# Performance work log

Measured on AMD Instinct MI355X. Metric: run time of the kernel, lower is better.

The kernel has to match this reference:

```python
import jax, jax.numpy as jnp
import numpy as np

B, N, D, H = 8, 8192, 512, 8  # batch, seq, hidden, heads
DH = D // H


def _rope_tables(n, d, dtype=jnp.float32):
    # standard rotate-half RoPE tables over the full hidden dim (d/2 freq pairs)
    half = d // 2
    inv_freq = 1.0 / (10000.0 ** (np.arange(0, half, dtype=np.float32) / half))
    pos = np.arange(n, dtype=np.float32)
    ang = np.einsum('n,f->nf', pos, inv_freq)          # [N, D/2]
    ang = np.concatenate([ang, ang], axis=-1)          # [N, D]
    return jnp.asarray(np.cos(ang), dtype), jnp.asarray(np.sin(ang), dtype)


def setup_inputs() -> dict:
    key = jax.random.key(0)
    k1, k2 = jax.random.split(key)
    hidden_states = jax.random.normal(k1, (B, N, D), dtype=jnp.float32)
    num_layers = 24
    std = 0.02 / np.sqrt(2.0 * num_layers * D)
    W = jax.random.normal(k2, (D, D), dtype=jnp.float32) * std
    cos, sin = _rope_tables(N, D)
    return {"hidden_states": hidden_states, "W": W, "cos": cos, "sin": sin}


def _rotate_half(x):
    x1, x2 = jnp.split(x, 2, axis=-1)
    return jnp.concatenate([-x2, x1], axis=-1)


def reference(hidden_states, W, cos, sin):
    # dropout(p=0) in eval mode -> identity
    x = hidden_states * cos + _rotate_half(hidden_states) * sin  # RoPE, [B,N,D]
    q = jnp.einsum('bnd,ed->bne', x, W)                          # F.linear(x, W)
    qh = q.reshape(B, N, H, DH)
    xh = x.reshape(B, N, H, DH)
    # linear-complexity path: (K^T V) then Q @ (.), per head
    kv = jnp.einsum('bnhd,bnhe->bhde', xh, xh)   # [B,H,DH,DH]
    out = jnp.einsum('bnhd,bhde->bnhe', qh, kv)  # [B,N,H,DH]
    return out.reshape(B, N, D)
```

## Files before the change

### kernel.cpp

```cpp
#include <hip/hip_runtime.h>
#include <hip/hip_bf16.h>
#include <stdint.h>

#define BB 8
#define NN 8192
#define DD 512
#define HH 8
#define DHD 64

typedef __attribute__((ext_vector_type(8))) short bf16x8;
typedef __attribute__((ext_vector_type(4))) float f32x4;

__device__ __forceinline__ unsigned short f2bf(float f) {
  union { float f; unsigned int u; } v; v.f = f;
  return (unsigned short)((v.u + 0x7FFFu + ((v.u >> 16) & 1u)) >> 16);
}

__device__ __forceinline__ void async16(const void* g, void* l) {
  __builtin_amdgcn_global_load_lds(
      (const __attribute__((address_space(1))) void*)g,
      (__attribute__((address_space(3))) void*)l, 16, 0, 0);
}

__global__ void rope_kernel(const float* __restrict__ h, const float* __restrict__ cs,
                            const float* __restrict__ sn, unsigned short* __restrict__ x) {
  int t = blockIdx.x * 256 + threadIdx.x;
  int r = t >> 6;
  int c = (t & 63) << 2;
  int n = r & (NN - 1);
  size_t base  = (size_t)r * DD + c;
  size_t tbase = (size_t)n * DD + c;
  float4 h1 = *(const float4*)(h + base);
  float4 h2 = *(const float4*)(h + base + 256);
  float4 c1 = *(const float4*)(cs + tbase);
  float4 c2 = *(const float4*)(cs + tbase + 256);
  float4 s1 = *(const float4*)(sn + tbase);
  float4 s2 = *(const float4*)(sn + tbase + 256);
  float4 x1, x2;
  x1.x = h1.x * c1.x - h2.x * s1.x;  x2.x = h2.x * c2.x + h1.x * s2.x;
  x1.y = h1.y * c1.y - h2.y * s1.y;  x2.y = h2.y * c2.y + h1.y * s2.y;
  x1.z = h1.z * c1.z - h2.z * s1.z;  x2.z = h2.z * c2.z + h1.z * s2.z;
  x1.w = h1.w * c1.w - h2.w * s1.w;  x2.w = h2.w * c2.w + h1.w * s2.w;
  uint2 p1, p2;
  p1.x = (unsigned)f2bf(x1.x) | ((unsigned)f2bf(x1.y) << 16);
  p1.y = (unsigned)f2bf(x1.z) | ((unsigned)f2bf(x1.w) << 16);
  p2.x = (unsigned)f2bf(x2.x) | ((unsigned)f2bf(x2.y) << 16);
  p2.y = (unsigned)f2bf(x2.z) | ((unsigned)f2bf(x2.w) << 16);
  *(uint2*)(x + base)       = p1;
  *(uint2*)(x + base + 256) = p2;
}

__global__ void kv_kernel(const unsigned short* __restrict__ x, float* __restrict__ kv) {
  __shared__ __align__(16) unsigned short xt[64 * 72];
  int bh = blockIdx.x;
  int b = bh >> 3, hh = bh & 7;
  int chunk = blockIdx.y;
  int rows_per_chunk = NN / gridDim.y;
  int tiles = rows_per_chunk >> 6;
  int tid = threadIdx.x;
  int wave = tid >> 6, lane = tid & 63;
  int d0 = (wave & 1) * 32, e0 = (wave >> 1) * 32;
  int l15 = lane & 15, q = lane >> 4;
  f32x4 acc[2][2];
#pragma unroll
  for (int i = 0; i < 2; ++i)
#pragma unroll
    for (int j = 0; j < 2; ++j) acc[i][j] = (f32x4){0.f, 0.f, 0.f, 0.f};

  int nrow = tid >> 2;
  int cseg = (tid & 3) * 16;
  const unsigned short* srcbase = x + (size_t)b * NN * DD + hh * DHD + cseg;

  for (int t = 0; t < tiles; ++t) {
    int n0 = chunk * rows_per_chunk + t * 64;
    const unsigned short* src = srcbase + (size_t)(n0 + nrow) * DD;
    uint4 p0 = *(const uint4*)(src);
    uint4 p1 = *(const uint4*)(src + 8);
    unsigned short v[16];
    *(uint4*)&v[0] = p0;  *(uint4*)&v[8] = p1;
#pragma unroll
    for (int j = 0; j < 16; ++j) xt[(cseg + j) * 72 + nrow] = v[j];
    __syncthreads();
#pragma unroll
    for (int ks = 0; ks < 64; ks += 32) {
      bf16x8 a0 = *(const bf16x8*)&xt[(d0 + l15) * 72 + ks + q * 8];
      bf16x8 a1 = *(const bf16x8*)&xt[(d0 + 16 + l15) * 72 + ks + q * 8];
      bf16x8 b0 = *(const bf16x8*)&xt[(e0 + l15) * 72 + ks + q * 8];
      bf16x8 b1 = *(const bf16x8*)&xt[(e0 + 16 + l15) * 72 + ks + q * 8];
      acc[0][0] = __builtin_amdgcn_mfma_f32_16x16x32_bf16(a0, b0, acc[0][0], 0, 0, 0);
      acc[1][0] = __builtin_amdgcn_mfma_f32_16x16x32_bf16(a1, b0, acc[1][0], 0, 0, 0);
      acc[0][1] = __builtin_amdgcn_mfma_f32_16x16x32_bf16(a0, b1, acc[0][1], 0, 0, 0);
      acc[1][1] = __builtin_amdgcn_mfma_f32_16x16x32_bf16(a1, b1, acc[1][1], 0, 0, 0);
    }
    __syncthreads();
  }
  float* dst = kv + (size_t)bh * 4096;
#pragma unroll
  for (int i = 0; i < 2; ++i)
#pragma unroll
    for (int j = 0; j < 2; ++j) {
      int col = e0 + j * 16 + l15;
#pragma unroll
      for (int reg = 0; reg < 4; ++reg) {
        int row = d0 + i * 16 + q * 4 + reg;
        atomicAdd(&dst[row * 64 + col], acc[i][j][reg]);
      }
    }
}

__global__ void wkvt_kernel(const float* __restrict__ W, const float* __restrict__ kv,
                            unsigned short* __restrict__ wkvt) {
  __shared__ float kvs[4096];
  __shared__ float ws[8192];
  int bh = blockIdx.x, fc = blockIdx.y;
  int b = bh >> 3, hh = bh & 7;
  int f0 = fc * 128;
  int tid = threadIdx.x;
#pragma unroll
  for (int i = 0; i < 4; ++i) {
    int idx = i * 1024 + tid * 4;
    *(float4*)&kvs[idx] = *(const float4*)&kv[(size_t)bh * 4096 + idx];
  }
#pragma unroll
  for (int i = 0; i < 8; ++i) {
    int idx = i * 1024 + tid * 4;
    int d = idx >> 7, f = idx & 127;
    *(float4*)&ws[idx] = *(const float4*)&W[(size_t)(hh * DHD + d) * DD + f0 + f];
  }
  __syncthreads();
  int e = tid & 63, fg = tid >> 6;
  float acc[32];
#pragma unroll
  for (int j = 0; j < 32; ++j) acc[j] = 0.f;
  for (int d = 0; d < 64; ++d) {
    float kvv = kvs[d * 64 + e];
    const float* wr = &ws[d * 128 + fg * 32];
#pragma unroll
    for (int j = 0; j < 32; ++j) acc[j] = fmaf(wr[j], kvv, acc[j]);
  }
  unsigned short tmp[32];
#pragma unroll
  for (int j = 0; j < 32; ++j) tmp[j] = f2bf(acc[j]);
  size_t obase = ((size_t)(b * DD + hh * DHD + e)) * DD + f0 + fg * 32;
#pragma unroll
  for (int qq = 0; qq < 4; ++qq)
    *(uint4*)&wkvt[obase + qq * 8] = *(uint4*)&tmp[qq * 8];
}

__global__ __launch_bounds__(256) void gemm_kernel(const unsigned short* __restrict__ x,
                                                   const unsigned short* __restrict__ wkvt,
                                                   float* __restrict__ out) {
  __shared__ __align__(16) unsigned short As[128 * 64];
  __shared__ __align__(16) unsigned short Bs[128 * 64];
  int mt = blockIdx.x, ct = blockIdx.y, bz = blockIdx.z;
  int tid = threadIdx.x, wave = tid >> 6, lane = tid & 63;
  int m_off = (wave & 1) * 64, c_off = (wave >> 1) * 64;
  int l15 = lane & 15, q = lane >> 4;
  int lrow = lane >> 3, lcol = (lane & 7) * 8;
  const unsigned short* Ag = x    + ((size_t)bz * NN + mt * 128) * DD;
  const unsigned short* Bg = wkvt + ((size_t)bz * DD + ct * 128) * DD;
  f32x4 acc[4][4];
#pragma unroll
  for (int i = 0; i < 4; ++i)
#pragma unroll
    for (int j = 0; j < 4; ++j) acc[i][j] = (f32x4){0.f, 0.f, 0.f, 0.f};

  for (int kk = 0; kk < 512; kk += 64) {
#pragma unroll
    for (int i = 0; i < 4; ++i) {
      int r = wave * 32 + i * 8 + lrow;
      async16(Ag + (size_t)r * DD + kk + lcol, &As[(wave * 32 + i * 8) * 64]);
      async16(Bg + (size_t)r * DD + kk + lcol, &Bs[(wave * 32 + i * 8) * 64]);
    }
    __syncthreads();
#pragma unroll
    for (int ks = 0; ks < 64; ks += 32) {
      bf16x8 a[4], bb[4];
#pragma unroll
      for (int i = 0; i < 4; ++i)
        a[i] = *(const bf16x8*)&As[(m_off + i * 16 + l15) * 64 + ks + q * 8];
#pragma unroll
      for (int j = 0; j < 4; ++j)
        bb[j] = *(const bf16x8*)&Bs[(c_off + j * 16 + l15) * 64 + ks + q * 8];
#pragma unroll
      for (int i = 0; i < 4; ++i)
#pragma unroll
        for (int j = 0; j < 4; ++j)
          acc[i][j] = __builtin_amdgcn_mfma_f32_16x16x32_bf16(a[i], bb[j], acc[i][j], 0, 0, 0);
    }
    __syncthreads();
  }
  float* ob = out + ((size_t)bz * NN + mt * 128) * DD + ct * 128;
#pragma unroll
  for (int i = 0; i < 4; ++i)
#pragma unroll
    for (int j = 0; j < 4; ++j) {
      int row = m_off + i * 16 + q * 4;
      int col = c_off + j * 16 + l15;
#pragma unroll
      for (int reg = 0; reg < 4; ++reg)
        ob[(size_t)(row + reg) * DD + col] = acc[i][j][reg];
    }
}

extern "C" void kernel_launch(void* const* d_in, const int* in_sizes, int n_in,
                              void* d_out, int out_size, void* d_ws, size_t ws_size,
                              hipStream_t stream) {
  (void)in_sizes; (void)n_in; (void)out_size;
  const float* h  = (const float*)d_in[0];
  const float* W  = (const float*)d_in[1];
  const float* cs = (const float*)d_in[2];
  const float* sn = (const float*)d_in[3];
  float* out = (float*)d_out;

  const size_t x_full     = (size_t)BB * NN * DD * 2;
  const size_t kv_full    = (size_t)BB * HH * DHD * DHD * 4;
  const size_t wkvt_full  = (size_t)BB * DD * DD * 2;
  const size_t x_batch    = (size_t)NN * DD * 2;
  const size_t kv_batch   = (size_t)HH * DHD * DHD * 4;
  const size_t wkvt_batch = (size_t)DD * DD * 2;

  if (ws_size >= x_full + kv_full + wkvt_full) {
    unsigned short* xw   = (unsigned short*)d_ws;
    float*          kv   = (float*)((char*)d_ws + x_full);
    unsigned short* wkvt = (unsigned short*)((char*)d_ws + x_full + kv_full);
    hipMemsetAsync(kv, 0, kv_full, stream);
    rope_kernel<<<dim3(BB * NN * 64 / 256), dim3(256), 0, stream>>>(h, cs, sn, xw);
    kv_kernel<<<dim3(BB * HH, 8), dim3(256), 0, stream>>>(xw, kv);
    wkvt_kernel<<<dim3(BB * HH, 4), dim3(256), 0, stream>>>(W, kv, wkvt);
    gemm_kernel<<<dim3(NN / 128, DD / 128, BB), dim3(256), 0, stream>>>(xw, wkvt, out);
  } else {
    unsigned short* xw   = (unsigned short*)d_ws;
    float*          kv   = (float*)((char*)d_ws + x_batch);
    unsigned short* wkvt = (unsigned short*)((char*)d_ws + x_batch + kv_batch);
    for (int b = 0; b < BB; ++b) {
      hipMemsetAsync(kv, 0, kv_batch, stream);
      rope_kernel<<<dim3(NN * 64 / 256), dim3(256), 0, stream>>>(
          h + (size_t)b * NN * DD, cs, sn, xw);
      kv_kernel<<<dim3(HH, 32), dim3(256), 0, stream>>>(xw, kv);
      wkvt_kernel<<<dim3(HH, 4), dim3(256), 0, stream>>>(W, kv, wkvt);
      gemm_kernel<<<dim3(NN / 128, DD / 128, 1), dim3(256), 0, stream>>>(
          xw, wkvt, out + (size_t)b * NN * DD);
    }
  }
}
```

Measured before the change: 337.6 us.

## Replace KV atomics with partial buffers, widen GEMM tile, nontemporal RoPE loads

The KV reduction now writes per-chunk partial sums to a buffer, and the next kernel adds them up. This replaces the atomicAdd calls and the memset. The KV transpose staging is rebuilt to pack pairs of rows into 32-bit LDS stores with a new padding. The GEMM tile is widened to 128x256 with 32 accumulators per wave, which cuts repeated A-tile loads at the cost of register pressure and occupancy. RoPE uses nontemporal loads for the hidden-state input and vector arithmetic.

```diff
diff --git a/kernel.cpp b/kernel.cpp
--- a/kernel.cpp
+++ b/kernel.cpp
@@ -7,9 +7,11 @@
 #define DD 512
 #define HH 8
 #define DHD 64
+#define NCH 16
 
 typedef __attribute__((ext_vector_type(8))) short bf16x8;
 typedef __attribute__((ext_vector_type(4))) float f32x4;
+typedef __attribute__((ext_vector_type(4))) float f4v;
 
 __device__ __forceinline__ unsigned short f2bf(float f) {
   union { float f; unsigned int u; } v; v.f = f;
@@ -30,17 +32,14 @@
   int n = r & (NN - 1);
   size_t base  = (size_t)r * DD + c;
   size_t tbase = (size_t)n * DD + c;
-  float4 h1 = *(const float4*)(h + base);
-  float4 h2 = *(const float4*)(h + base + 256);
-  float4 c1 = *(const float4*)(cs + tbase);
-  float4 c2 = *(const float4*)(cs + tbase + 256);
-  float4 s1 = *(const float4*)(sn + tbase);
-  float4 s2 = *(const float4*)(sn + tbase + 256);
-  float4 x1, x2;
-  x1.x = h1.x * c1.x - h2.x * s1.x;  x2.x = h2.x * c2.x + h1.x * s2.x;
-  x1.y = h1.y * c1.y - h2.y * s1.y;  x2.y = h2.y * c2.y + h1.y * s2.y;
-  x1.z = h1.z * c1.z - h2.z * s1.z;  x2.z = h2.z * c2.z + h1.z * s2.z;
-  x1.w = h1.w * c1.w - h2.w * s1.w;  x2.w = h2.w * c2.w + h1.w * s2.w;
+  f4v h1 = __builtin_nontemporal_load((const f4v*)(h + base));
+  f4v h2 = __builtin_nontemporal_load((const f4v*)(h + base + 256));
+  f4v c1 = *(const f4v*)(cs + tbase);
+  f4v c2 = *(const f4v*)(cs + tbase + 256);
+  f4v s1 = *(const f4v*)(sn + tbase);
+  f4v s2 = *(const f4v*)(sn + tbase + 256);
+  f4v x1 = h1 * c1 - h2 * s1;
+  f4v x2 = h2 * c2 + h1 * s2;
   uint2 p1, p2;
   p1.x = (unsigned)f2bf(x1.x) | ((unsigned)f2bf(x1.y) << 16);
   p1.y = (unsigned)f2bf(x1.z) | ((unsigned)f2bf(x1.w) << 16);
@@ -50,13 +49,11 @@
   *(uint2*)(x + base + 256) = p2;
 }
 
-__global__ void kv_kernel(const unsigned short* __restrict__ x, float* __restrict__ kv) {
-  __shared__ __align__(16) unsigned short xt[64 * 72];
+__global__ void kv_kernel(const unsigned short* __restrict__ x, float* __restrict__ kvp) {
+  __shared__ __align__(16) unsigned short xt[64 * 68];
   int bh = blockIdx.x;
   int b = bh >> 3, hh = bh & 7;
   int chunk = blockIdx.y;
-  int rows_per_chunk = NN / gridDim.y;
-  int tiles = rows_per_chunk >> 6;
   int tid = threadIdx.x;
   int wave = tid >> 6, lane = tid & 63;
   int d0 = (wave & 1) * 32, e0 = (wave >> 1) * 32;
@@ -67,34 +64,37 @@
 #pragma unroll
     for (int j = 0; j < 2; ++j) acc[i][j] = (f32x4){0.f, 0.f, 0.f, 0.f};
 
-  int nrow = tid >> 2;
-  int cseg = (tid & 3) * 16;
-  const unsigned short* srcbase = x + (size_t)b * NN * DD + hh * DHD + cseg;
-
-  for (int t = 0; t < tiles; ++t) {
-    int n0 = chunk * rows_per_chunk + t * 64;
-    const unsigned short* src = srcbase + (size_t)(n0 + nrow) * DD;
-    uint4 p0 = *(const uint4*)(src);
-    uint4 p1 = *(const uint4*)(src + 8);
-    unsigned short v[16];
-    *(uint4*)&v[0] = p0;  *(uint4*)&v[8] = p1;
-#pragma unroll
-    for (int j = 0; j < 16; ++j) xt[(cseg + j) * 72 + nrow] = v[j];
+  int rp  = tid & 31;
+  int seg = tid >> 5;
+  const unsigned short* srcbase = x + (size_t)b * NN * DD + hh * DHD + seg * 8;
+
+  for (int t = 0; t < 8; ++t) {
+    int n0 = chunk * 512 + t * 64;
+    const unsigned short* s0 = srcbase + (size_t)(n0 + 2 * rp) * DD;
+    uint4 p0 = *(const uint4*)(s0);
+    uint4 p1 = *(const uint4*)(s0 + DD);
+    unsigned short a0[8], a1[8];
+    *(uint4*)a0 = p0;  *(uint4*)a1 = p1;
+    __syncthreads();
+#pragma unroll
+    for (int j = 0; j < 8; ++j) {
+      unsigned pack = (unsigned)a0[j] | ((unsigned)a1[j] << 16);
+      ((unsigned*)xt)[(seg * 8 + j) * 34 + rp] = pack;
+    }
     __syncthreads();
 #pragma unroll
     for (int ks = 0; ks < 64; ks += 32) {
-      bf16x8 a0 = *(const bf16x8*)&xt[(d0 + l15) * 72 + ks + q * 8];
-      bf16x8 a1 = *(const bf16x8*)&xt[(d0 + 16 + l15) * 72 + ks + q * 8];
-      bf16x8 b0 = *(const bf16x8*)&xt[(e0 + l15) * 72 + ks + q * 8];
-      bf16x8 b1 = *(const bf16x8*)&xt[(e0 + 16 + l15) * 72 + ks + q * 8];
-      acc[0][0] = __builtin_amdgcn_mfma_f32_16x16x32_bf16(a0, b0, acc[0][0], 0, 0, 0);
-      acc[1][0] = __builtin_amdgcn_mfma_f32_16x16x32_bf16(a1, b0, acc[1][0], 0, 0, 0);
-      acc[0][1] = __builtin_amdgcn_mfma_f32_16x16x32_bf16(a0, b1, acc[0][1], 0, 0, 0);
-      acc[1][1] = __builtin_amdgcn_mfma_f32_16x16x32_bf16(a1, b1, acc[1][1], 0, 0, 0);
-    }
-    __syncthreads();
-  }
-  float* dst = kv + (size_t)bh * 4096;
+      bf16x8 a0f = *(const bf16x8*)&xt[(d0 + l15) * 68 + ks + q * 8];
+      bf16x8 a1f = *(const bf16x8*)&xt[(d0 + 16 + l15) * 68 + ks + q * 8];
+      bf16x8 b0f = *(const bf16x8*)&xt[(e0 + l15) * 68 + ks + q * 8];
+      bf16x8 b1f = *(const bf16x8*)&xt[(e0 + 16 + l15) * 68 + ks + q * 8];
+      acc[0][0] = __builtin_amdgcn_mfma_f32_16x16x32_bf16(a0f, b0f, acc[0][0], 0, 0, 0);
+      acc[1][0] = __builtin_amdgcn_mfma_f32_16x16x32_bf16(a1f, b0f, acc[1][0], 0, 0, 0);
+      acc[0][1] = __builtin_amdgcn_mfma_f32_16x16x32_bf16(a0f, b1f, acc[0][1], 0, 0, 0);
+      acc[1][1] = __builtin_amdgcn_mfma_f32_16x16x32_bf16(a1f, b1f, acc[1][1], 0, 0, 0);
+    }
+  }
+  float* dst = kvp + ((size_t)chunk * gridDim.x + bh) * 4096;
 #pragma unroll
   for (int i = 0; i < 2; ++i)
 #pragma unroll
@@ -103,23 +103,27 @@
 #pragma unroll
       for (int reg = 0; reg < 4; ++reg) {
         int row = d0 + i * 16 + q * 4 + reg;
-        atomicAdd(&dst[row * 64 + col], acc[i][j][reg]);
+        dst[row * 64 + col] = acc[i][j][reg];
       }
     }
 }
 
-__global__ void wkvt_kernel(const float* __restrict__ W, const float* __restrict__ kv,
+__global__ void wkvt_kernel(const float* __restrict__ W, const float* __restrict__ kvp,
                             unsigned short* __restrict__ wkvt) {
   __shared__ float kvs[4096];
   __shared__ float ws[8192];
   int bh = blockIdx.x, fc = blockIdx.y;
+  int nbh = gridDim.x;
   int b = bh >> 3, hh = bh & 7;
   int f0 = fc * 128;
   int tid = threadIdx.x;
 #pragma unroll
   for (int i = 0; i < 4; ++i) {
     int idx = i * 1024 + tid * 4;
-    *(float4*)&kvs[idx] = *(const float4*)&kv[(size_t)bh * 4096 + idx];
+    f4v s = (f4v){0.f, 0.f, 0.f, 0.f};
+    for (int c = 0; c < NCH; ++c)
+      s += *(const f4v*)&kvp[((size_t)c * nbh + bh) * 4096 + idx];
+    *(f4v*)&kvs[idx] = s;
   }
 #pragma unroll
   for (int i = 0; i < 8; ++i) {
@@ -147,54 +151,56 @@
     *(uint4*)&wkvt[obase + qq * 8] = *(uint4*)&tmp[qq * 8];
 }
 
-__global__ __launch_bounds__(256) void gemm_kernel(const unsigned short* __restrict__ x,
-                                                   const unsigned short* __restrict__ wkvt,
-                                                   float* __restrict__ out) {
+__global__ __launch_bounds__(256, 2) void gemm_kernel(const unsigned short* __restrict__ x,
+                                                      const unsigned short* __restrict__ wkvt,
+                                                      float* __restrict__ out) {
   __shared__ __align__(16) unsigned short As[128 * 64];
-  __shared__ __align__(16) unsigned short Bs[128 * 64];
+  __shared__ __align__(16) unsigned short Bs[256 * 64];
   int mt = blockIdx.x, ct = blockIdx.y, bz = blockIdx.z;
   int tid = threadIdx.x, wave = tid >> 6, lane = tid & 63;
-  int m_off = (wave & 1) * 64, c_off = (wave >> 1) * 64;
+  int m_off = (wave & 1) * 64, c_off = (wave >> 1) * 128;
   int l15 = lane & 15, q = lane >> 4;
   int lrow = lane >> 3, lcol = (lane & 7) * 8;
   const unsigned short* Ag = x    + ((size_t)bz * NN + mt * 128) * DD;
-  const unsigned short* Bg = wkvt + ((size_t)bz * DD + ct * 128) * DD;
-  f32x4 acc[4][4];
+  const unsigned short* Bg = wkvt + ((size_t)bz * DD + ct * 256) * DD;
+  f32x4 acc[4][8];
 #pragma unroll
   for (int i = 0; i < 4; ++i)
 #pragma unroll
-    for (int j = 0; j < 4; ++j) acc[i][j] = (f32x4){0.f, 0.f, 0.f, 0.f};
+    for (int j = 0; j < 8; ++j) acc[i][j] = (f32x4){0.f, 0.f, 0.f, 0.f};
 
   for (int kk = 0; kk < 512; kk += 64) {
 #pragma unroll
-    for (int i = 0; i < 4; ++i) {
-      int r = wave * 32 + i * 8 + lrow;
-      async16(Ag + (size_t)r * DD + kk + lcol, &As[(wave * 32 + i * 8) * 64]);
-      async16(Bg + (size_t)r * DD + kk + lcol, &Bs[(wave * 32 + i * 8) * 64]);
-    }
+    for (int i = 0; i < 4; ++i)
+      async16(Ag + (size_t)(wave * 32 + i * 8 + lrow) * DD + kk + lcol,
+              &As[(wave * 32 + i * 8) * 64]);
+#pragma unroll
+    for (int i = 0; i < 8; ++i)
+      async16(Bg + (size_t)(wave * 64 + i * 8 + lrow) * DD + kk + lcol,
+              &Bs[(wave * 64 + i * 8) * 64]);
     __syncthreads();
 #pragma unroll
     for (int ks = 0; ks < 64; ks += 32) {
-      bf16x8 a[4], bb[4];
+      bf16x8 a[4], bb[8];
 #pragma unroll
       for (int i = 0; i < 4; ++i)
         a[i] = *(const bf16x8*)&As[(m_off + i * 16 + l15) * 64 + ks + q * 8];
 #pragma unroll
-      for (int j = 0; j < 4; ++j)
+      for (int j = 0; j < 8; ++j)
         bb[j] = *(const bf16x8*)&Bs[(c_off + j * 16 + l15) * 64 + ks + q * 8];
 #pragma unroll
       for (int i = 0; i < 4; ++i)
 #pragma unroll
-        for (int j = 0; j < 4; ++j)
+        for (int j = 0; j < 8; ++j)
           acc[i][j] = __builtin_amdgcn_mfma_f32_16x16x32_bf16(a[i], bb[j], acc[i][j], 0, 0, 0);
     }
     __syncthreads();
   }
-  float* ob = out + ((size_t)bz * NN + mt * 128) * DD + ct * 128;
+  float* ob = out + ((size_t)bz * NN + mt * 128) * DD + ct * 256;
 #pragma unroll
   for (int i = 0; i < 4; ++i)
 #pragma unroll
-    for (int j = 0; j < 4; ++j) {
+    for (int j = 0; j < 8; ++j) {
       int row = m_off + i * 16 + q * 4;
       int col = c_off + j * 16 + l15;
 #pragma unroll
@@ -214,32 +220,30 @@
   float* out = (float*)d_out;
 
   const size_t x_full     = (size_t)BB * NN * DD * 2;
-  const size_t kv_full    = (size_t)BB * HH * DHD * DHD * 4;
+  const size_t kvp_full   = (size_t)NCH * BB * HH * DHD * DHD * 4;
   const size_t wkvt_full  = (size_t)BB * DD * DD * 2;
   const size_t x_batch    = (size_t)NN * DD * 2;
-  const size_t kv_batch   = (size_t)HH * DHD * DHD * 4;
+  const size_t kvp_batch  = (size_t)NCH * HH * DHD * DHD * 4;
   const size_t wkvt_batch = (size_t)DD * DD * 2;
 
-  if (ws_size >= x_full + kv_full + wkvt_full) {
+  if (ws_size >= x_full + kvp_full + wkvt_full) {
     unsigned short* xw   = (unsigned short*)d_ws;
-    float*          kv   = (float*)((char*)d_ws + x_full);
-    unsigned short* wkvt = (unsigned short*)((char*)d_ws + x_full + kv_full);
-    hipMemsetAsync(kv, 0, kv_full, stream);
+    float*          kvp  = (float*)((char*)d_ws + x_full);
+    unsigned short* wkvt = (unsigned short*)((char*)d_ws + x_full + kvp_full);
     rope_kernel<<<dim3(BB * NN * 64 / 256), dim3(256), 0, stream>>>(h, cs, sn, xw);
-    kv_kernel<<<dim3(BB * HH, 8), dim3(256), 0, stream>>>(xw, kv);
-    wkvt_kernel<<<dim3(BB * HH, 4), dim3(256), 0, stream>>>(W, kv, wkvt);
-    gemm_kernel<<<dim3(NN / 128, DD / 128, BB), dim3(256), 0, stream>>>(xw, wkvt, out);
+    kv_kernel<<<dim3(BB * HH, NCH), dim3(256), 0, stream>>>(xw, kvp);
+    wkvt_kernel<<<dim3(BB * HH, 4), dim3(256), 0, stream>>>(W, kvp, wkvt);
+    gemm_kernel<<<dim3(NN / 128, DD / 256, BB), dim3(256), 0, stream>>>(xw, wkvt, out);
   } else {
     unsigned short* xw   = (unsigned short*)d_ws;
-    float*          kv   = (float*)((char*)d_ws + x_batch);
-    unsigned short* wkvt = (unsigned short*)((char*)d_ws + x_batch + kv_batch);
+    float*          kvp  = (float*)((char*)d_ws + x_batch);
+    unsigned short* wkvt = (unsigned short*)((char*)d_ws + x_batch + kvp_batch);
     for (int b = 0; b < BB; ++b) {
-      hipMemsetAsync(kv, 0, kv_batch, stream);
       rope_kernel<<<dim3(NN * 64 / 256), dim3(256), 0, stream>>>(
           h + (size_t)b * NN * DD, cs, sn, xw);
-      kv_kernel<<<dim3(HH, 32), dim3(256), 0, stream>>>(xw, kv);
-      wkvt_kernel<<<dim3(HH, 4), dim3(256), 0, stream>>>(W, kv, wkvt);
-      gemm_kernel<<<dim3(NN / 128, DD / 128, 1), dim3(256), 0, stream>>>(
+      kv_kernel<<<dim3(HH, NCH), dim3(256), 0, stream>>>(xw, kvp);
+      wkvt_kernel<<<dim3(HH, 4), dim3(256), 0, stream>>>(W, kvp, wkvt);
+      gemm_kernel<<<dim3(NN / 128, DD / 256, 1), dim3(256), 0, stream>>>(
           xw, wkvt, out + (size_t)b * NN * DD);
     }
   }
```

Result: no change. 334.3 us (-1.0%).
